# Optimization experiments

Measured on AMD Instinct MI355X. Metric: run time of the kernel, lower is better.

Reference implementation:

```python
import jax, jax.numpy as jnp
import numpy as np

N = 100000      # nodes
E = 1600000     # edges
D_IN = 128
D_H = 128
D_OUT = 128


def setup_inputs() -> dict:
    key = jax.random.key(0)
    k1, k2, k3, k4, k5, k6 = jax.random.split(key, 6)
    x = jax.random.normal(k1, (N, D_IN), dtype=jnp.float32)
    edge_index = jax.random.randint(k2, (2, E), 0, N, dtype=jnp.int32)
    # GCNConv params: glorot-ish scaled weights, zero bias (PyG default zeros bias)
    W1 = jax.random.normal(k3, (D_IN, D_H), dtype=jnp.float32) * (1.0 / np.sqrt(D_IN))
    b1 = jnp.zeros((D_H,), dtype=jnp.float32)
    W2 = jax.random.normal(k4, (D_H, D_OUT), dtype=jnp.float32) * (1.0 / np.sqrt(D_H))
    b2 = jnpps = jnp.zeros((D_OUT,), dtype=jnp.float32)
    return {"x": x, "edge_index": edge_index, "W1": W1, "b1": b1, "W2": W2, "b2": b2}


def _gcn_layer(x, edge_index, W, b):
    # PyG GCNConv with add_self_loops=True, symmetric normalization:
    # out = D^{-1/2} (A + I) D^{-1/2} (x W) + b, deg computed at target (col)
    n = x.shape[0]
    row, col = edge_index[0], edge_index[1]
    deg = jax.ops.segment_sum(jnp.ones(row.shape, dtype=x.dtype), col,
                              num_segments=n) + 1.0  # +1 for self-loop
    dinv = jax.lax.rsqrt(deg)                         # [N]
    h = x @ W                                         # [N, D_out]
    coef = dinv[row] * dinv[col]                      # [E]
    agg = jax.ops.segment_sum(h[row] * coef[:, None], col, num_segments=n)
    agg = agg + (dinv * dinv)[:, None] * h            # self-loop term
    return agg + b


def reference(x, edge_index, W1, b1, W2, b2):
    h = jax.nn.relu(_gcn_layer(x, edge_index, W1, b1))
    return _gcn_layer(h, edge_index, W2, b2)
```

## Files before the change

### kernel.cpp

```cpp
#include <hip/hip_runtime.h>
#include <hip/hip_bf16.h>

using bf16 = __hip_bfloat16;
typedef __attribute__((ext_vector_type(8))) short short8;
typedef __attribute__((ext_vector_type(4))) float floatx4;
typedef __attribute__((ext_vector_type(4))) unsigned int uint4v;
typedef __attribute__((ext_vector_type(4))) float float4v;

__device__ __forceinline__ float bf2f(unsigned int u) {
    union { unsigned int i; float f; } x; x.i = u << 16; return x.f;
}
__device__ __forceinline__ float bf2f_hi(unsigned int u) {
    union { unsigned int i; float f; } x; x.i = u & 0xffff0000u; return x.f;
}
__device__ __forceinline__ unsigned short f2bf(float f) {
    union { float f; unsigned int i; } x; x.f = f;
    unsigned int r = x.i + 0x7fffu + ((x.i >> 16) & 1u);
    return (unsigned short)(r >> 16);
}

#define TSHIFT 9
#define TNODES 512
#define NCHUNK 4096
#define EPT 16
#define KMAX 24

__global__ __launch_bounds__(256)
void prep_w(const float* __restrict__ W1, const float* __restrict__ W2,
            unsigned short* __restrict__ Wt, unsigned int* __restrict__ sent1,
            unsigned int* __restrict__ sent2, int* __restrict__ tileCur, int T) {
    if (blockIdx.x == 0 && threadIdx.x < 64) sent1[threadIdx.x] = 0u;
    if (blockIdx.x == 2 && threadIdx.x < 64) sent2[threadIdx.x] = 0u;
    if (blockIdx.x == 1 && threadIdx.x < T) tileCur[threadIdx.x] = 0;
    const int id = blockIdx.x * 256 + threadIdx.x;
    const int m = id >> 14;
    const int r = id & 16383;
    const int n = r >> 7, k = r & 127;
    const float* W = m ? W2 : W1;
    Wt[((size_t)m << 14) + n * 128 + k] = f2bf(W[(size_t)k * 128 + n]);
}

__global__ __launch_bounds__(256)
void scatter_tiles(const int* __restrict__ row, const int* __restrict__ col,
                   int* __restrict__ tileCur, int* __restrict__ tileBuf,
                   int E, int T, int tcap) {
    __shared__ int grouped[NCHUNK];
    __shared__ unsigned short tlOf[NCHUNK];
    __shared__ int cnt[256], lo[256], off[256], lcur[256];
    const int t = threadIdx.x;
    const int e0 = blockIdx.x * NCHUNK;
    const int valid = min(NCHUNK, E - e0);
    cnt[t] = 0; lcur[t] = 0;
    int cc[EPT];
    #pragma unroll
    for (int k = 0; k < EPT; ++k) {
        int i = t + k * 256;
        cc[k] = (i < valid) ? col[e0 + i] : -1;
    }
    __syncthreads();
    #pragma unroll
    for (int k = 0; k < EPT; ++k)
        if (cc[k] >= 0) atomicAdd(&cnt[(unsigned)cc[k] >> TSHIFT], 1);
    __syncthreads();
    if (t == 0) {
        int run = 0;
        for (int s = 0; s < T; ++s) { lo[s] = run; run += cnt[s]; }
    }
    __syncthreads();
    if (t < T) off[t] = atomicAdd(&tileCur[t], cnt[t]);
    #pragma unroll
    for (int k = 0; k < EPT; ++k) {
        if (cc[k] >= 0) {
            int c = cc[k];
            int tl = (unsigned)c >> TSHIFT;
            int slot = lo[tl] + atomicAdd(&lcur[tl], 1);
            grouped[slot] = ((c & (TNODES - 1)) << 17) | row[e0 + t + k * 256];
            tlOf[slot] = (unsigned short)tl;
        }
    }
    __syncthreads();
    for (int i = t; i < valid; i += 256) {
        int tl = tlOf[i];
        tileBuf[(size_t)tl * tcap + off[tl] + (i - lo[tl])] = grouped[i];
    }
}

__global__ __launch_bounds__(512)
void build_csr(const int* __restrict__ tileCur, const int* __restrict__ tileBuf,
               int* __restrict__ csr, int* __restrict__ rowptr,
               int* __restrict__ deg64, float* __restrict__ dinv,
               int N, int tcap) {
    __shared__ int deg[TNODES];
    __shared__ int offs[TNODES];
    __shared__ int wpart[8];
    const int t = threadIdx.x;
    const int lane = t & 63, w = t >> 6;
    const int tile = blockIdx.x;
    const int nbase = tile << TSHIFT;
    const int cnt = tileCur[tile];
    const int* buf = tileBuf + (size_t)tile * tcap;
    deg[t] = 0;
    __syncthreads();
    int pv[KMAX];
    #pragma unroll
    for (int k = 0; k < KMAX; ++k) {
        int i = t + k * 512;
        pv[k] = (i < cnt) ? buf[i] : -1;
    }
    #pragma unroll
    for (int k = 0; k < KMAX; ++k)
        if (pv[k] >= 0) atomicAdd(&deg[pv[k] >> 17], 1);
    __syncthreads();
    const int a0 = deg[t];
    int v = a0;
    #pragma unroll
    for (int d = 1; d < 64; d <<= 1) {
        int o = __shfl_up(v, d, 64);
        if (lane >= d) v += o;
    }
    if (lane == 63) wpart[w] = v;
    __syncthreads();
    int basev = 0;
    #pragma unroll
    for (int j = 0; j < 8; ++j)
        if (j < w) basev += wpart[j];
    const int tb = basev + v - a0;
    offs[t] = tb;
    const size_t gbase = (size_t)tile * tcap;
    const int node = nbase + t;
    if (node < N) {
        rowptr[node] = (int)(gbase + tb);
        deg64[node] = min(a0, 64);
        dinv[node] = rsqrtf((float)a0 + 1.0f);
    }
    deg[t] = 0;
    __syncthreads();
    #pragma unroll
    for (int k = 0; k < KMAX; ++k) {
        if (pv[k] >= 0) {
            int ln = pv[k] >> 17;
            int pos = offs[ln] + atomicAdd(&deg[ln], 1);
            csr[gbase + pos] = pv[k] & 0x1FFFF;
        }
    }
}

template <bool RELU, typename OutT>
__global__ __launch_bounds__(256)
void aggregate(const bf16* __restrict__ xin, const float* __restrict__ dinv,
               const int* __restrict__ deg64, const int* __restrict__ rowptr,
               const int* __restrict__ csr,
               const float* __restrict__ bias, OutT* __restrict__ aggout,
               int n) {
    const int wave = (blockIdx.x * blockDim.x + threadIdx.x) >> 6;
    const int lane = threadIdx.x & 63;
    if (wave >= n) return;
    const int c = wave;

    const int dg = deg64[c];
    const int base = rowptr[c];
    int idx = n;
    if (lane < dg)
        idx = __builtin_nontemporal_load(&csr[base + lane]);

    const int q = lane >> 4;
    const int s = lane & 15;
    const unsigned short* xq = (const unsigned short*)xin + s * 8;

    float acc[8] = {};
    for (int i = 0; i < dg; i += 16) {
        #pragma unroll
        for (int j = 0; j < 4; ++j) {
            const int e = i + 4 * j + q;
            const int se = __shfl(idx, e, 64);
            uint4 u = *reinterpret_cast<const uint4*>(xq + (size_t)se * 128);
            acc[0] += bf2f(u.x & 0xffffu); acc[1] += bf2f_hi(u.x);
            acc[2] += bf2f(u.y & 0xffffu); acc[3] += bf2f_hi(u.y);
            acc[4] += bf2f(u.z & 0xffffu); acc[5] += bf2f_hi(u.z);
            acc[6] += bf2f(u.w & 0xffffu); acc[7] += bf2f_hi(u.w);
        }
    }
    #pragma unroll
    for (int d = 0; d < 8; ++d) {
        acc[d] += __shfl(acc[d], lane ^ 16, 64);
        acc[d] += __shfl(acc[d], lane ^ 32, 64);
    }

    if (lane < 16) {
        const float wc = dinv[c];
        uint4 uc = *reinterpret_cast<const uint4*>(xq + (size_t)c * 128);
        float sf[8] = { bf2f(uc.x & 0xffffu), bf2f_hi(uc.x),
                        bf2f(uc.y & 0xffffu), bf2f_hi(uc.y),
                        bf2f(uc.z & 0xffffu), bf2f_hi(uc.z),
                        bf2f(uc.w & 0xffffu), bf2f_hi(uc.w) };
        const float4* bb4 = reinterpret_cast<const float4*>(bias + s * 8);
        float4 b0 = bb4[0], b1 = bb4[1];
        float r[8];
        r[0] = (acc[0] + sf[0]) * wc + b0.x;
        r[1] = (acc[1] + sf[1]) * wc + b0.y;
        r[2] = (acc[2] + sf[2]) * wc + b0.z;
        r[3] = (acc[3] + sf[3]) * wc + b0.w;
        r[4] = (acc[4] + sf[4]) * wc + b1.x;
        r[5] = (acc[5] + sf[5]) * wc + b1.y;
        r[6] = (acc[6] + sf[6]) * wc + b1.z;
        r[7] = (acc[7] + sf[7]) * wc + b1.w;
        if (RELU) {
            #pragma unroll
            for (int d = 0; d < 8; ++d) r[d] = fmaxf(r[d], 0.f);
        }
        if constexpr (sizeof(OutT) == 2) {
            uint4v u;
            u.x = ((unsigned)f2bf(r[1]) << 16) | f2bf(r[0]);
            u.y = ((unsigned)f2bf(r[3]) << 16) | f2bf(r[2]);
            u.z = ((unsigned)f2bf(r[5]) << 16) | f2bf(r[4]);
            u.w = ((unsigned)f2bf(r[7]) << 16) | f2bf(r[6]);
            __builtin_nontemporal_store(u,
                (uint4v*)((unsigned short*)aggout + (size_t)c * 128 + s * 8));
        } else {
            float4v v0 = { r[0], r[1], r[2], r[3] };
            float4v v1 = { r[4], r[5], r[6], r[7] };
            float4v* dst = (float4v*)((float*)aggout + (size_t)c * 128 + s * 8);
            __builtin_nontemporal_store(v0, dst);
            __builtin_nontemporal_store(v1, dst + 1);
        }
    }
}

#define WSTR 168
template <typename AT>
__launch_bounds__(256)
__global__ void gemm_mfma(const AT* __restrict__ A, const unsigned short* __restrict__ Wt,
                          const float* __restrict__ dinv,
                          bf16* __restrict__ out, int M) {
    __shared__ unsigned short sWt[128 * WSTR];
    const int t = threadIdx.x;
    const int row0 = blockIdx.x * 64;
    const int wv = t >> 6;
    const int L  = t & 63;
    const int q  = L >> 4;
    const int l16 = L & 15;
    const int myrow = row0 + wv * 16 + l16;

    short8 af[4];
    if constexpr (sizeof(AT) == 4) {
        const bool ok = myrow < M;
        const float* Af = (const float*)A + (size_t)myrow * 128 + q * 8;
        #pragma unroll
        for (int c = 0; c < 4; ++c) {
            float4 v0 = make_float4(0.f, 0.f, 0.f, 0.f);
            float4 v1 = make_float4(0.f, 0.f, 0.f, 0.f);
            if (ok) {
                v0 = *reinterpret_cast<const float4*>(Af + c * 32);
                v1 = *reinterpret_cast<const float4*>(Af + c * 32 + 4);
            }
            af[c][0] = (short)f2bf(v0.x); af[c][1] = (short)f2bf(v0.y);
            af[c][2] = (short)f2bf(v0.z); af[c][3] = (short)f2bf(v0.w);
            af[c][4] = (short)f2bf(v1.x); af[c][5] = (short)f2bf(v1.y);
            af[c][6] = (short)f2bf(v1.z); af[c][7] = (short)f2bf(v1.w);
        }
    } else {
        const int ridx = myrow < M ? myrow : M;
        const unsigned short* Ab = (const unsigned short*)A + (size_t)ridx * 128 + q * 8;
        #pragma unroll
        for (int c = 0; c < 4; ++c)
            af[c] = *reinterpret_cast<const short8*>(Ab + c * 32);
    }

    #pragma unroll
    for (int i = 0; i < 8; ++i) {
        int s = t + 256 * i;
        int nn = s >> 4, k0 = (s & 15) * 8;
        *reinterpret_cast<uint4*>(&sWt[nn * WSTR + k0]) =
            *reinterpret_cast<const uint4*>(&Wt[(size_t)nn * 128 + k0]);
    }
    __syncthreads();

    floatx4 acc[8] = {};
    #pragma unroll
    for (int c = 0; c < 4; ++c) {
        #pragma unroll
        for (int nt = 0; nt < 8; ++nt) {
            short8 b = *reinterpret_cast<const short8*>(&sWt[(nt * 16 + l16) * WSTR + c * 32 + q * 8]);
            acc[nt] = __builtin_amdgcn_mfma_f32_16x16x32_bf16(af[c], b, acc[nt], 0, 0, 0);
        }
    }

    float dv[4];
    #pragma unroll
    for (int i = 0; i < 4; ++i) {
        int r = wv * 16 + q * 4 + i;
        dv[i] = (row0 + r < M) ? dinv[row0 + r] : 1.f;
    }
    __syncthreads();
    unsigned short* sOut = sWt;
    #pragma unroll
    for (int nt = 0; nt < 8; ++nt) {
        #pragma unroll
        for (int i = 0; i < 4; ++i) {
            int r = wv * 16 + q * 4 + i;
            sOut[r * 128 + nt * 16 + l16] = f2bf(acc[nt][i] * dv[i]);
        }
    }
    __syncthreads();
    #pragma unroll
    for (int i = 0; i < 4; ++i) {
        int idx = t + 256 * i;
        int r = idx >> 4, c8 = (idx & 15) * 8;
        if (row0 + r < M)
            *reinterpret_cast<uint4*>(out + (size_t)(row0 + r) * 128 + c8) =
                *reinterpret_cast<const uint4*>(&sOut[r * 128 + c8]);
    }
}

extern "C" void kernel_launch(void* const* d_in, const int* in_sizes, int n_in,
                              void* d_out, int out_size, void* d_ws, size_t ws_size,
                              hipStream_t stream) {
    const float* x  = (const float*)d_in[0];
    const int*   ei = (const int*)d_in[1];
    const float* W1 = (const float*)d_in[2];
    const float* b1 = (const float*)d_in[3];
    const float* W2 = (const float*)d_in[4];
    const float* b2 = (const float*)d_in[5];
    float* out = (float*)d_out;

    const int N = in_sizes[0] / 128;
    const int E = in_sizes[1] / 2;
    const int* row = ei;
    const int* col = ei + E;

    const int T = (N + TNODES - 1) >> TSHIFT;
    const int meanT = (E + T - 1) / T;
    int tcap = meanT + meanT / 8 + 1024;
    if (tcap > KMAX * TNODES) tcap = KMAX * TNODES;

    char* ws = (char*)d_ws;
    size_t off = 0;
    auto alloc = [&](size_t bytes) {
        void* p = ws + off;
        off += (bytes + 255) & ~(size_t)255;
        return p;
    };
    int*   tileCur = (int*)alloc((size_t)T * 4);
    int*   tileBuf = (int*)alloc((size_t)T * tcap * 4);
    int*   csr     = (int*)alloc((size_t)T * tcap * 4);
    int*   rowptr  = (int*)alloc((size_t)N * 4);
    int*   deg64   = (int*)alloc((size_t)N * 4);
    float* dinv    = (float*)alloc((size_t)N * 4);
    unsigned short* Wt = (unsigned short*)alloc(2 * 16384 * 2);
    bf16*  ha_bf   = (bf16*)alloc((size_t)(N + 1) * 128 * 2);
    bf16*  h1_bf   = (bf16*)alloc((size_t)(N + 1) * 128 * 2);

    prep_w<<<128, 256, 0, stream>>>(W1, W2, Wt,
                                    (unsigned int*)(ha_bf + (size_t)N * 128),
                                    (unsigned int*)(h1_bf + (size_t)N * 128),
                                    tileCur, T);
    scatter_tiles<<<(E + NCHUNK - 1) / NCHUNK, 256, 0, stream>>>(
        row, col, tileCur, tileBuf, E, T, tcap);
    build_csr<<<T, TNODES, 0, stream>>>(tileCur, tileBuf, csr, rowptr,
                                        deg64, dinv, N, tcap);

    const int aggBlocks = (int)(((size_t)N * 64 + 255) / 256);
    const int gemmBlocks = (N + 63) / 64;

    gemm_mfma<float><<<gemmBlocks, 256, 0, stream>>>(x, Wt, dinv, ha_bf, N);
    aggregate<true, bf16><<<aggBlocks, 256, 0, stream>>>(ha_bf, dinv, deg64, rowptr, csr, b1, h1_bf, N);

    gemm_mfma<bf16><<<gemmBlocks, 256, 0, stream>>>(h1_bf, Wt + 16384, dinv, ha_bf, N);
    aggregate<false, float><<<aggBlocks, 256, 0, stream>>>(ha_bf, dinv, deg64, rowptr, csr, b2, out, N);
}
```

Measured before the change: 289.7 us.

## Fuse layer-1 aggregation with layer-2 GEMM in one kernel

Adds an agg_gemm kernel. Each 1024-thread block aggregates neighbor features for 64 nodes, applying bias and ReLU, stages the bf16 result in shared memory, then runs the layer-2 MFMA GEMM with dinv scaling directly from LDS. This removes one kernel launch and the global write and read of the intermediate h1 activations. In exchange it uses large 1024-thread blocks with heavy LDS use, which may reduce occupancy and latency hiding for the irregular gather.

```diff
diff --git a/kernel.cpp b/kernel.cpp
--- a/kernel.cpp
+++ b/kernel.cpp
@@ -142,6 +142,138 @@
             int pos = offs[ln] + atomicAdd(&deg[ln], 1);
             csr[gbase + pos] = pv[k] & 0x1FFFF;
         }
+    }
+}
+
+#define WSTR 168
+
+__global__ __launch_bounds__(1024)
+void agg_gemm(const bf16* __restrict__ xin, const float* __restrict__ dinv,
+              const int* __restrict__ deg64, const int* __restrict__ rowptr,
+              const int* __restrict__ csr, const float* __restrict__ bias,
+              const unsigned short* __restrict__ Wt,
+              bf16* __restrict__ out, int n) {
+    __shared__ unsigned short sWt[128 * WSTR];
+    __shared__ unsigned short sX[64 * WSTR];
+    const int t = threadIdx.x;
+    const int w = t >> 6, lane = t & 63;
+    const int row0 = blockIdx.x * 64;
+
+    #pragma unroll
+    for (int i = 0; i < 2; ++i) {
+        int sl = t + 1024 * i;
+        int nn = sl >> 4, k0 = (sl & 15) * 8;
+        *reinterpret_cast<uint4*>(&sWt[nn * WSTR + k0]) =
+            *reinterpret_cast<const uint4*>(&Wt[(size_t)nn * 128 + k0]);
+    }
+
+    const int q = lane >> 4;
+    const int s = lane & 15;
+    const unsigned short* xq = (const unsigned short*)xin + s * 8;
+    #pragma unroll
+    for (int j = 0; j < 4; ++j) {
+        const int slot = w * 4 + j;
+        const int c = row0 + slot;
+        if (c >= n) {
+            if (lane < 16) {
+                uint4v z = { 0u, 0u, 0u, 0u };
+                *reinterpret_cast<uint4v*>(&sX[slot * WSTR + s * 8]) = z;
+            }
+            continue;
+        }
+        const int dg = deg64[c];
+        const int base = rowptr[c];
+        int idx = n;
+        if (lane < dg)
+            idx = __builtin_nontemporal_load(&csr[base + lane]);
+        float acc[8] = {};
+        for (int i = 0; i < dg; i += 16) {
+            #pragma unroll
+            for (int jj = 0; jj < 4; ++jj) {
+                const int e = i + 4 * jj + q;
+                const int se = __shfl(idx, e, 64);
+                uint4 u = *reinterpret_cast<const uint4*>(xq + (size_t)se * 128);
+                acc[0] += bf2f(u.x & 0xffffu); acc[1] += bf2f_hi(u.x);
+                acc[2] += bf2f(u.y & 0xffffu); acc[3] += bf2f_hi(u.y);
+                acc[4] += bf2f(u.z & 0xffffu); acc[5] += bf2f_hi(u.z);
+                acc[6] += bf2f(u.w & 0xffffu); acc[7] += bf2f_hi(u.w);
+            }
+        }
+        #pragma unroll
+        for (int d = 0; d < 8; ++d) {
+            acc[d] += __shfl(acc[d], lane ^ 16, 64);
+            acc[d] += __shfl(acc[d], lane ^ 32, 64);
+        }
+        if (lane < 16) {
+            const float wc = dinv[c];
+            uint4 uc = *reinterpret_cast<const uint4*>(xq + (size_t)c * 128);
+            float sf[8] = { bf2f(uc.x & 0xffffu), bf2f_hi(uc.x),
+                            bf2f(uc.y & 0xffffu), bf2f_hi(uc.y),
+                            bf2f(uc.z & 0xffffu), bf2f_hi(uc.z),
+                            bf2f(uc.w & 0xffffu), bf2f_hi(uc.w) };
+            const float4* bb4 = reinterpret_cast<const float4*>(bias + s * 8);
+            float4 b0 = bb4[0], b1 = bb4[1];
+            float r[8];
+            r[0] = fmaxf((acc[0] + sf[0]) * wc + b0.x, 0.f);
+            r[1] = fmaxf((acc[1] + sf[1]) * wc + b0.y, 0.f);
+            r[2] = fmaxf((acc[2] + sf[2]) * wc + b0.z, 0.f);
+            r[3] = fmaxf((acc[3] + sf[3]) * wc + b0.w, 0.f);
+            r[4] = fmaxf((acc[4] + sf[4]) * wc + b1.x, 0.f);
+            r[5] = fmaxf((acc[5] + sf[5]) * wc + b1.y, 0.f);
+            r[6] = fmaxf((acc[6] + sf[6]) * wc + b1.z, 0.f);
+            r[7] = fmaxf((acc[7] + sf[7]) * wc + b1.w, 0.f);
+            uint4v u;
+            u.x = ((unsigned)f2bf(r[1]) << 16) | f2bf(r[0]);
+            u.y = ((unsigned)f2bf(r[3]) << 16) | f2bf(r[2]);
+            u.z = ((unsigned)f2bf(r[5]) << 16) | f2bf(r[4]);
+            u.w = ((unsigned)f2bf(r[7]) << 16) | f2bf(r[6]);
+            *reinterpret_cast<uint4v*>(&sX[slot * WSTR + s * 8]) = u;
+        }
+    }
+    __syncthreads();
+
+    const int wr = w >> 2, wc = w & 3;
+    const int l16 = lane & 15, qq = lane >> 4;
+    short8 af[4];
+    #pragma unroll
+    for (int c4 = 0; c4 < 4; ++c4)
+        af[c4] = *reinterpret_cast<const short8*>(
+            &sX[(wr * 16 + l16) * WSTR + c4 * 32 + qq * 8]);
+    floatx4 acc2[2] = {};
+    #pragma unroll
+    for (int c4 = 0; c4 < 4; ++c4) {
+        #pragma unroll
+        for (int ntl = 0; ntl < 2; ++ntl) {
+            const int nt = wc * 2 + ntl;
+            short8 b = *reinterpret_cast<const short8*>(
+                &sWt[(nt * 16 + l16) * WSTR + c4 * 32 + qq * 8]);
+            acc2[ntl] = __builtin_amdgcn_mfma_f32_16x16x32_bf16(af[c4], b, acc2[ntl], 0, 0, 0);
+        }
+    }
+
+    float dv[4];
+    #pragma unroll
+    for (int i = 0; i < 4; ++i) {
+        int r = wr * 16 + qq * 4 + i;
+        dv[i] = (row0 + r < n) ? dinv[row0 + r] : 1.f;
+    }
+    __syncthreads();
+    unsigned short* sOut = sWt;
+    #pragma unroll
+    for (int ntl = 0; ntl < 2; ++ntl) {
+        #pragma unroll
+        for (int i = 0; i < 4; ++i) {
+            int r = wr * 16 + qq * 4 + i;
+            int col = wc * 32 + ntl * 16 + l16;
+            sOut[r * 128 + col] = f2bf(acc2[ntl][i] * dv[i]);
+        }
+    }
+    __syncthreads();
+    {
+        int r = t >> 4, c8 = (t & 15) * 8;
+        if (row0 + r < n)
+            *reinterpret_cast<uint4*>(out + (size_t)(row0 + r) * 128 + c8) =
+                *reinterpret_cast<const uint4*>(&sOut[r * 128 + c8]);
     }
 }
 
@@ -226,7 +358,6 @@
     }
 }
 
-#define WSTR 168
 template <typename AT>
 __launch_bounds__(256)
 __global__ void gemm_mfma(const AT* __restrict__ A, const unsigned short* __restrict__ Wt,
@@ -347,12 +478,12 @@
     int*   deg64   = (int*)alloc((size_t)N * 4);
     float* dinv    = (float*)alloc((size_t)N * 4);
     unsigned short* Wt = (unsigned short*)alloc(2 * 16384 * 2);
-    bf16*  ha_bf   = (bf16*)alloc((size_t)(N + 1) * 128 * 2);
-    bf16*  h1_bf   = (bf16*)alloc((size_t)(N + 1) * 128 * 2);
+    bf16*  hs1 = (bf16*)alloc((size_t)(N + 1) * 128 * 2);
+    bf16*  hs2 = (bf16*)alloc((size_t)(N + 1) * 128 * 2);
 
     prep_w<<<128, 256, 0, stream>>>(W1, W2, Wt,
-                                    (unsigned int*)(ha_bf + (size_t)N * 128),
-                                    (unsigned int*)(h1_bf + (size_t)N * 128),
+                                    (unsigned int*)(hs1 + (size_t)N * 128),
+                                    (unsigned int*)(hs2 + (size_t)N * 128),
                                     tileCur, T);
     scatter_tiles<<<(E + NCHUNK - 1) / NCHUNK, 256, 0, stream>>>(
         row, col, tileCur, tileBuf, E, T, tcap);
@@ -362,9 +493,8 @@
     const int aggBlocks = (int)(((size_t)N * 64 + 255) / 256);
     const int gemmBlocks = (N + 63) / 64;
 
-    gemm_mfma<float><<<gemmBlocks, 256, 0, stream>>>(x, Wt, dinv, ha_bf, N);
-    aggregate<true, bf16><<<aggBlocks, 256, 0, stream>>>(ha_bf, dinv, deg64, rowptr, csr, b1, h1_bf, N);
-
-    gemm_mfma<bf16><<<gemmBlocks, 256, 0, stream>>>(h1_bf, Wt + 16384, dinv, ha_bf, N);
-    aggregate<false, float><<<aggBlocks, 256, 0, stream>>>(ha_bf, dinv, deg64, rowptr, csr, b2, out, N);
-}
+    gemm_mfma<float><<<gemmBlocks, 256, 0, stream>>>(x, Wt, dinv, hs1, N);
+    agg_gemm<<<gemmBlocks, 1024, 0, stream>>>(hs1, dinv, deg64, rowptr, csr,
+                                              b1, Wt + 16384, hs2, N);
+    aggregate<false, float><<<aggBlocks, 256, 0, stream>>>(hs2, dinv, deg64, rowptr, csr, b2, out, N);
+}
```

After: 289.5 us. No clear change (-0.1%).
